# Performance work log

Measured on AMD Instinct MI355X. Metric: run time of the kernel, lower is better.

## Reference

```python
import jax, jax.numpy as jnp
import numpy as np

N_NODES = 100000

def _glorot(key, shape):
    lim = np.sqrt(6.0 / (shape[0] + shape[1])).astype(np.float32)
    return jax.random.uniform(key, shape, jnp.float32, -lim, lim)

def setup_inputs() -> dict:
    key = jax.random.key(0)
    ks = jax.random.split(key, 9)
    x = jax.random.normal(ks[0], (N_NODES, 256), jnp.float32)
    edge_index = jax.random.randint(ks[1], (2, 1600000), 0, N_NODES, jnp.int32)
    dims = [(256, 256), (256, 256), (256, 40)]
    params = {}
    for i, (din, dout) in enumerate(dims):
        params[f"Wl{i}"] = _glorot(ks[2 + 2 * i], (din, dout))   # neighbor (lin_l) weight
        params[f"Wr{i}"] = _glorot(ks[3 + 2 * i], (din, dout))   # root (lin_r) weight
        params[f"b{i}"] = jnp.zeros((dout,), jnp.float32)
    return {"x": x, "edge_index": edge_index, **params}

def _sage_conv(x, src, dst, Wl, Wr, b):
    # mean-aggregate neighbor features at destination nodes, then linear
    msg_sum = jax.ops.segment_sum(x[src], dst, num_segments=N_NODES)      # [N, d]
    deg = jax.ops.segment_sum(jnp.ones((src.shape[0],), x.dtype), dst,
                              num_segments=N_NODES)                       # [N]
    mean = msg_sum / jnp.maximum(deg, 1.0)[:, None]
    return mean @ Wl + x @ Wr + b

def reference(x, edge_index, Wl0, Wr0, b0, Wl1, Wr1, b1, Wl2, Wr2, b2):
    src, dst = edge_index[0], edge_index[1]
    h = jax.nn.relu(_sage_conv(x, src, dst, Wl0, Wr0, b0))
    h = jax.nn.relu(_sage_conv(h, src, dst, Wl1, Wr1, b1))
    h = _sage_conv(h, src, dst, Wl2, Wr2, b2)
    return jax.nn.log_softmax(h, axis=1)
```

## Files before the change

kernel.cpp:

```cpp
#include <hip/hip_runtime.h>
#include <hip/hip_bf16.h>
#include <math.h>

#define N_NODES 100000
#define N_EDGES 1600000
#define DIN 256
#define KTOT 512
#define SLOTS 64

typedef __attribute__((ext_vector_type(8))) short frag_ab;
typedef __attribute__((ext_vector_type(4))) float frag_cd;

__device__ inline unsigned short f2bf(float f) {
    union { float f; unsigned u; } v; v.f = f;
    unsigned r = v.u + 0x7FFF + ((v.u >> 16) & 1);
    return (unsigned short)(r >> 16);
}
__device__ inline float bf2f(unsigned u16) {
    union { unsigned u; float f; } v; v.u = u16 << 16;
    return v.f;
}
__device__ inline float bf_lo(unsigned u) {
    union { unsigned u; float f; } v; v.u = u << 16; return v.f;
}
__device__ inline float bf_hi(unsigned u) {
    union { unsigned u; float f; } v; v.u = u & 0xffff0000u; return v.f;
}

__global__ void build_bucket(const int* __restrict__ src, const int* __restrict__ dst,
                             int* __restrict__ cnt, int* __restrict__ col, int nE) {
    int e = blockIdx.x * blockDim.x + threadIdx.x;
    if (e >= nE) return;
    int d = dst[e];
    int pos = atomicAdd(&cnt[d], 1);
    if (pos < SLOTS) col[(size_t)d * SLOTS + pos] = src[e];
}

__global__ void conv_f32_bf16(const float* __restrict__ x, unsigned short* __restrict__ y, int n4) {
    int i = blockIdx.x * blockDim.x + threadIdx.x;
    if (i >= n4) return;
    float4 v = ((const float4*)x)[i];
    uint2 o;
    o.x = (unsigned)f2bf(v.x) | ((unsigned)f2bf(v.y) << 16);
    o.y = (unsigned)f2bf(v.z) | ((unsigned)f2bf(v.w) << 16);
    ((uint2*)y)[i] = o;
}

__global__ void conv_weights(const float* __restrict__ Wl0, const float* __restrict__ Wr0,
                             const float* __restrict__ Wl1, const float* __restrict__ Wr1,
                             const float* __restrict__ Wl2, const float* __restrict__ Wr2,
                             unsigned short* __restrict__ Wt0, unsigned short* __restrict__ Wt1,
                             unsigned short* __restrict__ Wl2t, unsigned short* __restrict__ Wr2t) {
    int idx = blockIdx.x * blockDim.x + threadIdx.x;
    if (idx < 262144) {
        const float* Wl = (idx < 131072) ? Wl0 : Wl1;
        const float* Wr = (idx < 131072) ? Wr0 : Wr1;
        unsigned short* Wt = (idx < 131072) ? Wt0 : Wt1;
        int i = idx & 131071;
        int n = i >> 9, k = i & 511;
        float v = (k < 256) ? Wl[k * 256 + n] : Wr[(k - 256) * 256 + n];
        Wt[i] = f2bf(v);
    } else if (idx < 294912) {
        const float* W = (idx < 278528) ? Wl2 : Wr2;
        unsigned short* Wt = (idx < 278528) ? Wl2t : Wr2t;
        int i = (idx - 262144) & 16383;
        int n = i >> 8, k = i & 255;
        Wt[i] = f2bf((n < 40) ? W[k * 40 + n] : 0.f);
    }
}

__global__ __launch_bounds__(256) void gather_mean_bf(
    const int* __restrict__ cnt, const int* __restrict__ col,
    const unsigned short* __restrict__ h, unsigned short* __restrict__ mean, int nNodes) {
    int node = blockIdx.x * 4 + (threadIdx.x >> 6);
    int lane = threadIdx.x & 63;
    if (node >= nNodes) return;
    int deg = cnt[node];
    int nd = (deg < SLOTS) ? deg : SLOTS;
    const int* cp = col + (size_t)node * SLOTS;
    int half = lane >> 5;
    int l = lane & 31;
    float a0 = 0, a1 = 0, a2 = 0, a3 = 0, a4 = 0, a5 = 0, a6 = 0, a7 = 0;
    int e = 0;
    for (; e + 8 <= nd; e += 8) {
        int s0 = cp[e + half];
        int s1 = cp[e + 2 + half];
        int s2 = cp[e + 4 + half];
        int s3 = cp[e + 6 + half];
        uint4 v0 = *(const uint4*)(h + (size_t)s0 * DIN + l * 8);
        uint4 v1 = *(const uint4*)(h + (size_t)s1 * DIN + l * 8);
        uint4 v2 = *(const uint4*)(h + (size_t)s2 * DIN + l * 8);
        uint4 v3 = *(const uint4*)(h + (size_t)s3 * DIN + l * 8);
        a0 += bf_lo(v0.x); a1 += bf_hi(v0.x); a2 += bf_lo(v0.y); a3 += bf_hi(v0.y);
        a4 += bf_lo(v0.z); a5 += bf_hi(v0.z); a6 += bf_lo(v0.w); a7 += bf_hi(v0.w);
        a0 += bf_lo(v1.x); a1 += bf_hi(v1.x); a2 += bf_lo(v1.y); a3 += bf_hi(v1.y);
        a4 += bf_lo(v1.z); a5 += bf_hi(v1.z); a6 += bf_lo(v1.w); a7 += bf_hi(v1.w);
        a0 += bf_lo(v2.x); a1 += bf_hi(v2.x); a2 += bf_lo(v2.y); a3 += bf_hi(v2.y);
        a4 += bf_lo(v2.z); a5 += bf_hi(v2.z); a6 += bf_lo(v2.w); a7 += bf_hi(v2.w);
        a0 += bf_lo(v3.x); a1 += bf_hi(v3.x); a2 += bf_lo(v3.y); a3 += bf_hi(v3.y);
        a4 += bf_lo(v3.z); a5 += bf_hi(v3.z); a6 += bf_lo(v3.w); a7 += bf_hi(v3.w);
    }
    for (; e + 2 <= nd; e += 2) {
        int s = cp[e + half];
        uint4 v = *(const uint4*)(h + (size_t)s * DIN + l * 8);
        a0 += bf_lo(v.x); a1 += bf_hi(v.x); a2 += bf_lo(v.y); a3 += bf_hi(v.y);
        a4 += bf_lo(v.z); a5 += bf_hi(v.z); a6 += bf_lo(v.w); a7 += bf_hi(v.w);
    }
    if (e < nd && half == 0) {
        int s = cp[e];
        uint4 v = *(const uint4*)(h + (size_t)s * DIN + l * 8);
        a0 += bf_lo(v.x); a1 += bf_hi(v.x); a2 += bf_lo(v.y); a3 += bf_hi(v.y);
        a4 += bf_lo(v.z); a5 += bf_hi(v.z); a6 += bf_lo(v.w); a7 += bf_hi(v.w);
    }
    a0 += __shfl_xor(a0, 32); a1 += __shfl_xor(a1, 32);
    a2 += __shfl_xor(a2, 32); a3 += __shfl_xor(a3, 32);
    a4 += __shfl_xor(a4, 32); a5 += __shfl_xor(a5, 32);
    a6 += __shfl_xor(a6, 32); a7 += __shfl_xor(a7, 32);
    if (half == 0) {
        float inv = 1.0f / fmaxf((float)deg, 1.0f);
        uint4 o;
        o.x = (unsigned)f2bf(a0 * inv) | ((unsigned)f2bf(a1 * inv) << 16);
        o.y = (unsigned)f2bf(a2 * inv) | ((unsigned)f2bf(a3 * inv) << 16);
        o.z = (unsigned)f2bf(a4 * inv) | ((unsigned)f2bf(a5 * inv) << 16);
        o.w = (unsigned)f2bf(a6 * inv) | ((unsigned)f2bf(a7 * inv) << 16);
        *(uint4*)(mean + (size_t)node * DIN + l * 8) = o;
    }
}

__global__ __launch_bounds__(256) void gather_mean64(
    const int* __restrict__ cnt, const int* __restrict__ col,
    const unsigned short* __restrict__ z, unsigned short* __restrict__ mz, int nNodes) {
    int node = blockIdx.x * 4 + (threadIdx.x >> 6);
    int lane = threadIdx.x & 63;
    if (node >= nNodes) return;
    int deg = cnt[node];
    int nd = (deg < SLOTS) ? deg : SLOTS;
    const int* cp = col + (size_t)node * SLOTS;
    int g = lane >> 4;
    int l = lane & 15;
    float a0 = 0, a1 = 0, a2 = 0, a3 = 0;
    int e = 0;
    for (; e + 8 <= nd; e += 8) {
        int s0 = cp[e + g];
        int s1 = cp[e + 4 + g];
        uint2 v0 = *(const uint2*)(z + (size_t)s0 * 64 + l * 4);
        uint2 v1 = *(const uint2*)(z + (size_t)s1 * 64 + l * 4);
        a0 += bf_lo(v0.x); a1 += bf_hi(v0.x); a2 += bf_lo(v0.y); a3 += bf_hi(v0.y);
        a0 += bf_lo(v1.x); a1 += bf_hi(v1.x); a2 += bf_lo(v1.y); a3 += bf_hi(v1.y);
    }
    for (; e + 4 <= nd; e += 4) {
        int s = cp[e + g];
        uint2 v = *(const uint2*)(z + (size_t)s * 64 + l * 4);
        a0 += bf_lo(v.x); a1 += bf_hi(v.x); a2 += bf_lo(v.y); a3 += bf_hi(v.y);
    }
    int rem = nd - e;
    if (g < rem) {
        int s = cp[e + g];
        uint2 v = *(const uint2*)(z + (size_t)s * 64 + l * 4);
        a0 += bf_lo(v.x); a1 += bf_hi(v.x); a2 += bf_lo(v.y); a3 += bf_hi(v.y);
    }
    a0 += __shfl_xor(a0, 16); a1 += __shfl_xor(a1, 16);
    a2 += __shfl_xor(a2, 16); a3 += __shfl_xor(a3, 16);
    a0 += __shfl_xor(a0, 32); a1 += __shfl_xor(a1, 32);
    a2 += __shfl_xor(a2, 32); a3 += __shfl_xor(a3, 32);
    if (lane < 16) {
        float inv = 1.0f / fmaxf((float)deg, 1.0f);
        uint2 o;
        o.x = (unsigned)f2bf(a0 * inv) | ((unsigned)f2bf(a1 * inv) << 16);
        o.y = (unsigned)f2bf(a2 * inv) | ((unsigned)f2bf(a3 * inv) << 16);
        *(uint2*)(mz + (size_t)node * 64 + l * 4) = o;
    }
}

template <bool RELU>
__global__ __launch_bounds__(256) void sage_mfma(
    const unsigned short* __restrict__ mean, const unsigned short* __restrict__ h,
    const unsigned short* __restrict__ Wt, const float* __restrict__ bias,
    unsigned short* __restrict__ out, int nNodes) {
    __shared__ unsigned short sA[64][32];
    __shared__ unsigned short sB[256][32];

    int tid = threadIdx.x;
    int wave = tid >> 6;
    int lane = tid & 63;
    int lrow = lane & 15;
    int quad = lane >> 4;
    int node0 = blockIdx.x * 64;

    frag_cd acc[4][4];
#pragma unroll
    for (int mi = 0; mi < 4; mi++)
#pragma unroll
        for (int ni = 0; ni < 4; ni++) acc[mi][ni] = (frag_cd){0.f, 0.f, 0.f, 0.f};

    int ar = tid >> 2;
    int ak = (tid & 3) * 8;
    int aNode = node0 + ar;

    for (int kb = 0; kb < KTOT; kb += 32) {
        {
            const unsigned short* srcp = (kb < 256)
                ? (mean + (size_t)aNode * DIN + kb + ak)
                : (h + (size_t)aNode * DIN + (kb - 256) + ak);
            uint4 av = {0u, 0u, 0u, 0u};
            if (aNode < nNodes) av = *(const uint4*)srcp;
            *(uint4*)(&sA[ar][ak]) = av;
        }
        {
            const unsigned short* wp = Wt + (size_t)tid * KTOT + kb;
#pragma unroll
            for (int j = 0; j < 4; j++)
                *(uint4*)(&sB[tid][j * 8]) = *(const uint4*)(wp + j * 8);
        }
        __syncthreads();

        frag_ab aF[4], bF[4];
#pragma unroll
        for (int mi = 0; mi < 4; mi++)
            aF[mi] = *(const frag_ab*)(&sA[mi * 16 + lrow][quad * 8]);
#pragma unroll
        for (int ni = 0; ni < 4; ni++)
            bF[ni] = *(const frag_ab*)(&sB[(wave * 4 + ni) * 16 + lrow][quad * 8]);

#pragma unroll
        for (int mi = 0; mi < 4; mi++)
#pragma unroll
            for (int ni = 0; ni < 4; ni++)
                acc[mi][ni] = __builtin_amdgcn_mfma_f32_16x16x32_bf16(
                    aF[mi], bF[ni], acc[mi][ni], 0, 0, 0);
        __syncthreads();
    }

#pragma unroll
    for (int ni = 0; ni < 4; ni++) {
        int colc = (wave * 4 + ni) * 16 + lrow;
        float bv = bias[colc];
#pragma unroll
        for (int mi = 0; mi < 4; mi++) {
#pragma unroll
            for (int r = 0; r < 4; r++) {
                int node = node0 + mi * 16 + quad * 4 + r;
                if (node < nNodes) {
                    float v = acc[mi][ni][r] + bv;
                    if (RELU) v = fmaxf(v, 0.f);
                    out[(size_t)node * 256 + colc] = f2bf(v);
                }
            }
        }
    }
}

__global__ __launch_bounds__(256) void mfma_lin64(
    const unsigned short* __restrict__ h, const unsigned short* __restrict__ Wt,
    unsigned short* __restrict__ z, int nNodes) {
    __shared__ unsigned short sA[64][32];
    __shared__ unsigned short sB[64][32];

    int tid = threadIdx.x;
    int wave = tid >> 6;
    int lane = tid & 63;
    int lrow = lane & 15;
    int quad = lane >> 4;
    int node0 = blockIdx.x * 64;

    frag_cd acc[4];
#pragma unroll
    for (int ni = 0; ni < 4; ni++) acc[ni] = (frag_cd){0.f, 0.f, 0.f, 0.f};

    int ar = tid >> 2;
    int ak = (tid & 3) * 8;
    int aNode = node0 + ar;

    for (int kb = 0; kb < 256; kb += 32) {
        uint4 av = {0u, 0u, 0u, 0u};
        if (aNode < nNodes) av = *(const uint4*)(h + (size_t)aNode * DIN + kb + ak);
        *(uint4*)(&sA[ar][ak]) = av;
        *(uint4*)(&sB[ar][ak]) = *(const uint4*)(Wt + (size_t)ar * 256 + kb + ak);
        __syncthreads();

        frag_ab aF = *(const frag_ab*)(&sA[wave * 16 + lrow][quad * 8]);
#pragma unroll
        for (int ni = 0; ni < 4; ni++) {
            frag_ab bF = *(const frag_ab*)(&sB[ni * 16 + lrow][quad * 8]);
            acc[ni] = __builtin_amdgcn_mfma_f32_16x16x32_bf16(aF, bF, acc[ni], 0, 0, 0);
        }
        __syncthreads();
    }

#pragma unroll
    for (int ni = 0; ni < 4; ni++) {
        int colc = ni * 16 + lrow;
#pragma unroll
        for (int r = 0; r < 4; r++) {
            int node = node0 + wave * 16 + quad * 4 + r;
            if (node < nNodes)
                z[(size_t)node * 64 + colc] = f2bf(acc[ni][r]);
        }
    }
}

__global__ __launch_bounds__(256) void sage_out(
    const unsigned short* __restrict__ h, const unsigned short* __restrict__ Wt,
    const unsigned short* __restrict__ mz, const float* __restrict__ bias,
    float* __restrict__ out, int nNodes) {
    __shared__ unsigned short sA[64][32];
    __shared__ unsigned short sB[64][32];

    int tid = threadIdx.x;
    int wave = tid >> 6;
    int lane = tid & 63;
    int lrow = lane & 15;
    int quad = lane >> 4;
    int node0 = blockIdx.x * 64;

    frag_cd acc[4];
#pragma unroll
    for (int ni = 0; ni < 4; ni++) acc[ni] = (frag_cd){0.f, 0.f, 0.f, 0.f};

    int ar = tid >> 2;
    int ak = (tid & 3) * 8;
    int aNode = node0 + ar;

    for (int kb = 0; kb < 256; kb += 32) {
        uint4 av = {0u, 0u, 0u, 0u};
        if (aNode < nNodes) av = *(const uint4*)(h + (size_t)aNode * DIN + kb + ak);
        *(uint4*)(&sA[ar][ak]) = av;
        *(uint4*)(&sB[ar][ak]) = *(const uint4*)(Wt + (size_t)ar * 256 + kb + ak);
        __syncthreads();

        frag_ab aF = *(const frag_ab*)(&sA[wave * 16 + lrow][quad * 8]);
#pragma unroll
        for (int ni = 0; ni < 4; ni++) {
            frag_ab bF = *(const frag_ab*)(&sB[ni * 16 + lrow][quad * 8]);
            acc[ni] = __builtin_amdgcn_mfma_f32_16x16x32_bf16(aF, bF, acc[ni], 0, 0, 0);
        }
        __syncthreads();
    }

#pragma unroll
    for (int r = 0; r < 4; r++) {
        int node = node0 + wave * 16 + quad * 4 + r;
        bool valid = (node < nNodes);
        float v[4];
#pragma unroll
        for (int ni = 0; ni < 4; ni++) {
            int colc = ni * 16 + lrow;
            if (colc < 40 && valid)
                v[ni] = acc[ni][r] + bias[colc] + bf2f(mz[(size_t)node * 64 + colc]);
            else
                v[ni] = -INFINITY;
        }
        float m = fmaxf(fmaxf(v[0], v[1]), fmaxf(v[2], v[3]));
#pragma unroll
        for (int off = 1; off < 16; off <<= 1) m = fmaxf(m, __shfl_xor(m, off));
        float s = 0.f;
#pragma unroll
        for (int ni = 0; ni < 4; ni++)
            if (v[ni] != -INFINITY) s += expf(v[ni] - m);
#pragma unroll
        for (int off = 1; off < 16; off <<= 1) s += __shfl_xor(s, off);
        float ls = logf(s);
#pragma unroll
        for (int ni = 0; ni < 4; ni++) {
            int colc = ni * 16 + lrow;
            if (valid && colc < 40)
                out[(size_t)node * 40 + colc] = v[ni] - m - ls;
        }
    }
}

extern "C" void kernel_launch(void* const* d_in, const int* in_sizes, int n_in,
                              void* d_out, int out_size, void* d_ws, size_t ws_size,
                              hipStream_t stream) {
    const float* x   = (const float*)d_in[0];
    const int*   ei  = (const int*)d_in[1];
    const float* Wl0 = (const float*)d_in[2];
    const float* Wr0 = (const float*)d_in[3];
    const float* b0  = (const float*)d_in[4];
    const float* Wl1 = (const float*)d_in[5];
    const float* Wr1 = (const float*)d_in[6];
    const float* b1  = (const float*)d_in[7];
    const float* Wl2 = (const float*)d_in[8];
    const float* Wr2 = (const float*)d_in[9];
    const float* b2  = (const float*)d_in[10];
    float* out = (float*)d_out;

    const int* src = ei;
    const int* dst = ei + N_EDGES;

    const size_t NODE_PAD = 100352;
    char* ws = (char*)d_ws;
    int* cnt  = (int*)ws;  ws += NODE_PAD * sizeof(int);
    int* colv = (int*)ws;  ws += (size_t)NODE_PAD * SLOTS * sizeof(int);
    unsigned short* xbf  = (unsigned short*)ws; ws += (size_t)N_NODES * DIN * sizeof(unsigned short);
    unsigned short* mean = (unsigned short*)ws; ws += (size_t)N_NODES * DIN * sizeof(unsigned short);
    unsigned short* h1   = (unsigned short*)ws; ws += (size_t)N_NODES * DIN * sizeof(unsigned short);
    unsigned short* h2   = (unsigned short*)ws; ws += (size_t)N_NODES * DIN * sizeof(unsigned short);
    unsigned short* zb   = (unsigned short*)ws; ws += (size_t)N_NODES * 64 * sizeof(unsigned short);
    unsigned short* mz   = (unsigned short*)ws; ws += (size_t)N_NODES * 64 * sizeof(unsigned short);
    unsigned short* Wt0  = (unsigned short*)ws; ws += 256 * KTOT * sizeof(unsigned short);
    unsigned short* Wt1  = (unsigned short*)ws; ws += 256 * KTOT * sizeof(unsigned short);
    unsigned short* Wl2t = (unsigned short*)ws; ws += 64 * 256 * sizeof(unsigned short);
    unsigned short* Wr2t = (unsigned short*)ws; ws += 64 * 256 * sizeof(unsigned short);

    hipMemsetAsync(cnt, 0, N_NODES * sizeof(int), stream);
    build_bucket<<<(N_EDGES + 255) / 256, 256, 0, stream>>>(src, dst, cnt, colv, N_EDGES);

    conv_f32_bf16<<<(N_NODES * DIN / 4 + 255) / 256, 256, 0, stream>>>(x, xbf, N_NODES * DIN / 4);
    conv_weights<<<(294912 + 255) / 256, 256, 0, stream>>>(Wl0, Wr0, Wl1, Wr1, Wl2, Wr2,
                                                           Wt0, Wt1, Wl2t, Wr2t);

    const int gatherBlocks = (N_NODES + 3) / 4;
    const int mfmaBlocks = (N_NODES + 63) / 64;

    gather_mean_bf<<<gatherBlocks, 256, 0, stream>>>(cnt, colv, xbf, mean, N_NODES);
    sage_mfma<true><<<mfmaBlocks, 256, 0, stream>>>(mean, xbf, Wt0, b0, h1, N_NODES);

    gather_mean_bf<<<gatherBlocks, 256, 0, stream>>>(cnt, colv, h1, mean, N_NODES);
    sage_mfma<true><<<mfmaBlocks, 256, 0, stream>>>(mean, h1, Wt1, b1, h2, N_NODES);

    mfma_lin64<<<mfmaBlocks, 256, 0, stream>>>(h2, Wl2t, zb, N_NODES);
    gather_mean64<<<gatherBlocks, 256, 0, stream>>>(cnt, colv, zb, mz, N_NODES);
    sage_out<<<mfmaBlocks, 256, 0, stream>>>(h2, Wr2t, mz, b2, out, N_NODES);
}
```

Measured before the change: 777.4 us.

## Fuse prep kernels, unroll gather by 16, and double MFMA tile to 128 rows

Merges the edge bucketing, weight conversion and feature bf16 conversion into one prep launch, partitioned by block index. Adds a 16-edge unrolled loop in the mean gather so more independent row loads are in flight per wave. Enlarges the layer GEMM block to 128 nodes with 512 threads (8 waves split 2x4), so each loaded weight tile is reused across twice as many rows. This trades higher shared memory and register use per block, and fewer blocks in the grid, for fewer launches and less weight reloading.

```diff
diff --git a/kernel.cpp b/kernel.cpp
--- a/kernel.cpp
+++ b/kernel.cpp
@@ -27,47 +27,51 @@
     union { unsigned u; float f; } v; v.u = u & 0xffff0000u; return v.f;
 }
 
-__global__ void build_bucket(const int* __restrict__ src, const int* __restrict__ dst,
-                             int* __restrict__ cnt, int* __restrict__ col, int nE) {
-    int e = blockIdx.x * blockDim.x + threadIdx.x;
-    if (e >= nE) return;
-    int d = dst[e];
-    int pos = atomicAdd(&cnt[d], 1);
-    if (pos < SLOTS) col[(size_t)d * SLOTS + pos] = src[e];
-}
-
-__global__ void conv_f32_bf16(const float* __restrict__ x, unsigned short* __restrict__ y, int n4) {
-    int i = blockIdx.x * blockDim.x + threadIdx.x;
-    if (i >= n4) return;
-    float4 v = ((const float4*)x)[i];
-    uint2 o;
-    o.x = (unsigned)f2bf(v.x) | ((unsigned)f2bf(v.y) << 16);
-    o.y = (unsigned)f2bf(v.z) | ((unsigned)f2bf(v.w) << 16);
-    ((uint2*)y)[i] = o;
-}
-
-__global__ void conv_weights(const float* __restrict__ Wl0, const float* __restrict__ Wr0,
-                             const float* __restrict__ Wl1, const float* __restrict__ Wr1,
-                             const float* __restrict__ Wl2, const float* __restrict__ Wr2,
-                             unsigned short* __restrict__ Wt0, unsigned short* __restrict__ Wt1,
-                             unsigned short* __restrict__ Wl2t, unsigned short* __restrict__ Wr2t) {
-    int idx = blockIdx.x * blockDim.x + threadIdx.x;
-    if (idx < 262144) {
-        const float* Wl = (idx < 131072) ? Wl0 : Wl1;
-        const float* Wr = (idx < 131072) ? Wr0 : Wr1;
-        unsigned short* Wt = (idx < 131072) ? Wt0 : Wt1;
-        int i = idx & 131071;
-        int n = i >> 9, k = i & 511;
-        float v = (k < 256) ? Wl[k * 256 + n] : Wr[(k - 256) * 256 + n];
-        Wt[i] = f2bf(v);
-    } else if (idx < 294912) {
-        const float* W = (idx < 278528) ? Wl2 : Wr2;
-        unsigned short* Wt = (idx < 278528) ? Wl2t : Wr2t;
-        int i = (idx - 262144) & 16383;
-        int n = i >> 8, k = i & 255;
-        Wt[i] = f2bf((n < 40) ? W[k * 40 + n] : 0.f);
-    }
-}
+__global__ __launch_bounds__(256) void prep(
+    const int* __restrict__ src, const int* __restrict__ dst,
+    int* __restrict__ cnt, int* __restrict__ col,
+    const float* __restrict__ x, unsigned short* __restrict__ xbf,
+    const float* __restrict__ Wl0, const float* __restrict__ Wr0,
+    const float* __restrict__ Wl1, const float* __restrict__ Wr1,
+    const float* __restrict__ Wl2, const float* __restrict__ Wr2,
+    unsigned short* __restrict__ Wt0, unsigned short* __restrict__ Wt1,
+    unsigned short* __restrict__ Wl2t, unsigned short* __restrict__ Wr2t) {
+    int b = blockIdx.x;
+    int tid = threadIdx.x;
+    if (b < 6250) {
+        int e = b * 256 + tid;
+        int d = dst[e];
+        int pos = atomicAdd(&cnt[d], 1);
+        if (pos < SLOTS) col[(size_t)d * SLOTS + pos] = src[e];
+    } else if (b < 7402) {
+        int idx = (b - 6250) * 256 + tid;
+        if (idx < 262144) {
+            const float* Wl = (idx < 131072) ? Wl0 : Wl1;
+            const float* Wr = (idx < 131072) ? Wr0 : Wr1;
+            unsigned short* Wt = (idx < 131072) ? Wt0 : Wt1;
+            int i = idx & 131071;
+            int n = i >> 9, k = i & 511;
+            float v = (k < 256) ? Wl[k * 256 + n] : Wr[(k - 256) * 256 + n];
+            Wt[i] = f2bf(v);
+        } else if (idx < 294912) {
+            const float* W = (idx < 278528) ? Wl2 : Wr2;
+            unsigned short* Wt = (idx < 278528) ? Wl2t : Wr2t;
+            int i = (idx - 262144) & 16383;
+            int n = i >> 8, k = i & 255;
+            Wt[i] = f2bf((n < 40) ? W[k * 40 + n] : 0.f);
+        }
+    } else {
+        int i = (b - 7402) * 256 + tid;
+        float4 v = ((const float4*)x)[i];
+        uint2 o;
+        o.x = (unsigned)f2bf(v.x) | ((unsigned)f2bf(v.y) << 16);
+        o.y = (unsigned)f2bf(v.z) | ((unsigned)f2bf(v.w) << 16);
+        ((uint2*)xbf)[i] = o;
+    }
+}
+
+#define ACC8(v) { a0 += bf_lo(v.x); a1 += bf_hi(v.x); a2 += bf_lo(v.y); a3 += bf_hi(v.y); \
+                  a4 += bf_lo(v.z); a5 += bf_hi(v.z); a6 += bf_lo(v.w); a7 += bf_hi(v.w); }
 
 __global__ __launch_bounds__(256) void gather_mean_bf(
     const int* __restrict__ cnt, const int* __restrict__ col,
@@ -82,6 +86,25 @@
     int l = lane & 31;
     float a0 = 0, a1 = 0, a2 = 0, a3 = 0, a4 = 0, a5 = 0, a6 = 0, a7 = 0;
     int e = 0;
+    for (; e + 16 <= nd; e += 16) {
+        int s0 = cp[e + half];
+        int s1 = cp[e + 2 + half];
+        int s2 = cp[e + 4 + half];
+        int s3 = cp[e + 6 + half];
+        int s4 = cp[e + 8 + half];
+        int s5 = cp[e + 10 + half];
+        int s6 = cp[e + 12 + half];
+        int s7 = cp[e + 14 + half];
+        uint4 v0 = *(const uint4*)(h + (size_t)s0 * DIN + l * 8);
+        uint4 v1 = *(const uint4*)(h + (size_t)s1 * DIN + l * 8);
+        uint4 v2 = *(const uint4*)(h + (size_t)s2 * DIN + l * 8);
+        uint4 v3 = *(const uint4*)(h + (size_t)s3 * DIN + l * 8);
+        uint4 v4 = *(const uint4*)(h + (size_t)s4 * DIN + l * 8);
+        uint4 v5 = *(const uint4*)(h + (size_t)s5 * DIN + l * 8);
+        uint4 v6 = *(const uint4*)(h + (size_t)s6 * DIN + l * 8);
+        uint4 v7 = *(const uint4*)(h + (size_t)s7 * DIN + l * 8);
+        ACC8(v0) ACC8(v1) ACC8(v2) ACC8(v3) ACC8(v4) ACC8(v5) ACC8(v6) ACC8(v7)
+    }
     for (; e + 8 <= nd; e += 8) {
         int s0 = cp[e + half];
         int s1 = cp[e + 2 + half];
@@ -91,26 +114,17 @@
         uint4 v1 = *(const uint4*)(h + (size_t)s1 * DIN + l * 8);
         uint4 v2 = *(const uint4*)(h + (size_t)s2 * DIN + l * 8);
         uint4 v3 = *(const uint4*)(h + (size_t)s3 * DIN + l * 8);
-        a0 += bf_lo(v0.x); a1 += bf_hi(v0.x); a2 += bf_lo(v0.y); a3 += bf_hi(v0.y);
-        a4 += bf_lo(v0.z); a5 += bf_hi(v0.z); a6 += bf_lo(v0.w); a7 += bf_hi(v0.w);
-        a0 += bf_lo(v1.x); a1 += bf_hi(v1.x); a2 += bf_lo(v1.y); a3 += bf_hi(v1.y);
-        a4 += bf_lo(v1.z); a5 += bf_hi(v1.z); a6 += bf_lo(v1.w); a7 += bf_hi(v1.w);
-        a0 += bf_lo(v2.x); a1 += bf_hi(v2.x); a2 += bf_lo(v2.y); a3 += bf_hi(v2.y);
-        a4 += bf_lo(v2.z); a5 += bf_hi(v2.z); a6 += bf_lo(v2.w); a7 += bf_hi(v2.w);
-        a0 += bf_lo(v3.x); a1 += bf_hi(v3.x); a2 += bf_lo(v3.y); a3 += bf_hi(v3.y);
-        a4 += bf_lo(v3.z); a5 += bf_hi(v3.z); a6 += bf_lo(v3.w); a7 += bf_hi(v3.w);
+        ACC8(v0) ACC8(v1) ACC8(v2) ACC8(v3)
     }
     for (; e + 2 <= nd; e += 2) {
         int s = cp[e + half];
         uint4 v = *(const uint4*)(h + (size_t)s * DIN + l * 8);
-        a0 += bf_lo(v.x); a1 += bf_hi(v.x); a2 += bf_lo(v.y); a3 += bf_hi(v.y);
-        a4 += bf_lo(v.z); a5 += bf_hi(v.z); a6 += bf_lo(v.w); a7 += bf_hi(v.w);
+        ACC8(v)
     }
     if (e < nd && half == 0) {
         int s = cp[e];
         uint4 v = *(const uint4*)(h + (size_t)s * DIN + l * 8);
-        a0 += bf_lo(v.x); a1 += bf_hi(v.x); a2 += bf_lo(v.y); a3 += bf_hi(v.y);
-        a4 += bf_lo(v.z); a5 += bf_hi(v.z); a6 += bf_lo(v.w); a7 += bf_hi(v.w);
+        ACC8(v)
     }
     a0 += __shfl_xor(a0, 32); a1 += __shfl_xor(a1, 32);
     a2 += __shfl_xor(a2, 32); a3 += __shfl_xor(a3, 32);
@@ -172,12 +186,11 @@
     }
 }
 
-template <bool RELU>
-__global__ __launch_bounds__(256) void sage_mfma(
+__global__ __launch_bounds__(512) void sage_mfma(
     const unsigned short* __restrict__ mean, const unsigned short* __restrict__ h,
     const unsigned short* __restrict__ Wt, const float* __restrict__ bias,
     unsigned short* __restrict__ out, int nNodes) {
-    __shared__ unsigned short sA[64][32];
+    __shared__ unsigned short sA[128][32];
     __shared__ unsigned short sB[256][32];
 
     int tid = threadIdx.x;
@@ -185,7 +198,9 @@
     int lane = tid & 63;
     int lrow = lane & 15;
     int quad = lane >> 4;
-    int node0 = blockIdx.x * 64;
+    int node0 = blockIdx.x * 128;
+    int mg = wave & 1;
+    int ng = wave >> 1;
 
     frag_cd acc[4][4];
 #pragma unroll
@@ -196,6 +211,8 @@
     int ar = tid >> 2;
     int ak = (tid & 3) * 8;
     int aNode = node0 + ar;
+    int br = tid >> 1;
+    int bk = (tid & 1) * 16;
 
     for (int kb = 0; kb < KTOT; kb += 32) {
         {
@@ -207,20 +224,19 @@
             *(uint4*)(&sA[ar][ak]) = av;
         }
         {
-            const unsigned short* wp = Wt + (size_t)tid * KTOT + kb;
-#pragma unroll
-            for (int j = 0; j < 4; j++)
-                *(uint4*)(&sB[tid][j * 8]) = *(const uint4*)(wp + j * 8);
+            const unsigned short* wp = Wt + (size_t)br * KTOT + kb + bk;
+            *(uint4*)(&sB[br][bk]) = *(const uint4*)(wp);
+            *(uint4*)(&sB[br][bk + 8]) = *(const uint4*)(wp + 8);
         }
         __syncthreads();
 
         frag_ab aF[4], bF[4];
 #pragma unroll
         for (int mi = 0; mi < 4; mi++)
-            aF[mi] = *(const frag_ab*)(&sA[mi * 16 + lrow][quad * 8]);
+            aF[mi] = *(const frag_ab*)(&sA[(mg * 4 + mi) * 16 + lrow][quad * 8]);
 #pragma unroll
         for (int ni = 0; ni < 4; ni++)
-            bF[ni] = *(const frag_ab*)(&sB[(wave * 4 + ni) * 16 + lrow][quad * 8]);
+            bF[ni] = *(const frag_ab*)(&sB[(ng * 4 + ni) * 16 + lrow][quad * 8]);
 
 #pragma unroll
         for (int mi = 0; mi < 4; mi++)
@@ -233,16 +249,15 @@
 
 #pragma unroll
     for (int ni = 0; ni < 4; ni++) {
-        int colc = (wave * 4 + ni) * 16 + lrow;
+        int colc = (ng * 4 + ni) * 16 + lrow;
         float bv = bias[colc];
 #pragma unroll
         for (int mi = 0; mi < 4; mi++) {
 #pragma unroll
             for (int r = 0; r < 4; r++) {
-                int node = node0 + mi * 16 + quad * 4 + r;
+                int node = node0 + (mg * 4 + mi) * 16 + quad * 4 + r;
                 if (node < nNodes) {
-                    float v = acc[mi][ni][r] + bv;
-                    if (RELU) v = fmaxf(v, 0.f);
+                    float v = fmaxf(acc[mi][ni][r] + bv, 0.f);
                     out[(size_t)node * 256 + colc] = f2bf(v);
                 }
             }
@@ -404,22 +419,21 @@
     unsigned short* Wr2t = (unsigned short*)ws; ws += 64 * 256 * sizeof(unsigned short);
 
     hipMemsetAsync(cnt, 0, N_NODES * sizeof(int), stream);
-    build_bucket<<<(N_EDGES + 255) / 256, 256, 0, stream>>>(src, dst, cnt, colv, N_EDGES);
-
-    conv_f32_bf16<<<(N_NODES * DIN / 4 + 255) / 256, 256, 0, stream>>>(x, xbf, N_NODES * DIN / 4);
-    conv_weights<<<(294912 + 255) / 256, 256, 0, stream>>>(Wl0, Wr0, Wl1, Wr1, Wl2, Wr2,
-                                                           Wt0, Wt1, Wl2t, Wr2t);
-
-    const int gatherBlocks = (N_NODES + 3) / 4;
-    const int mfmaBlocks = (N_NODES + 63) / 64;
-
-    gather_mean_bf<<<gatherBlocks, 256, 0, stream>>>(cnt, colv, xbf, mean, N_NODES);
-    sage_mfma<true><<<mfmaBlocks, 256, 0, stream>>>(mean, xbf, Wt0, b0, h1, N_NODES);
-
-    gather_mean_bf<<<gatherBlocks, 256, 0, stream>>>(cnt, colv, h1, mean, N_NODES);
-    sage_mfma<true><<<mfmaBlocks, 256, 0, stream>>>(mean, h1, Wt1, b1, h2, N_NODES);
-
-    mfma_lin64<<<mfmaBlocks, 256, 0, stream>>>(h2, Wl2t, zb, N_NODES);
-    gather_mean64<<<gatherBlocks, 256, 0, stream>>>(cnt, colv, zb, mz, N_NODES);
-    sage_out<<<mfmaBlocks, 256, 0, stream>>>(h2, Wr2t, mz, b2, out, N_NODES);
-}
+    prep<<<32402, 256, 0, stream>>>(src, dst, cnt, colv, x, xbf,
+                                    Wl0, Wr0, Wl1, Wr1, Wl2, Wr2,
+                                    Wt0, Wt1, Wl2t, Wr2t);
+
+    const int nodeBlocks = (N_NODES + 3) / 4;
+    const int mfmaBlocks128 = (N_NODES + 127) / 128;
+    const int mfmaBlocks64 = (N_NODES + 63) / 64;
+
+    gather_mean_bf<<<nodeBlocks, 256, 0, stream>>>(cnt, colv, xbf, mean, N_NODES);
+    sage_mfma<<<mfmaBlocks128, 512, 0, stream>>>(mean, xbf, Wt0, b0, h1, N_NODES);
+
+    gather_mean_bf<<<nodeBlocks, 256, 0, stream>>>(cnt, colv, h1, mean, N_NODES);
+    sage_mfma<<<mfmaBlocks128, 512, 0, stream>>>(mean, h1, Wt1, b1, h2, N_NODES);
+
+    mfma_lin64<<<mfmaBlocks64, 256, 0, stream>>>(h2, Wl2t, zb, N_NODES);
+    gather_mean64<<<nodeBlocks, 256, 0, stream>>>(cnt, colv, zb, mz, N_NODES);
+    sage_out<<<mfmaBlocks64, 256, 0, stream>>>(h2, Wr2t, mz, b2, out, N_NODES);
+}
```

Result: faster. 715.2 us (-8.0%).
